# Kernel optimization log

Hardware: AMD Instinct MI355X
Metric: run time of the kernel (lower is better)

The kernel has to match this reference:

```python
import jax, jax.numpy as jnp
import numpy as np

D_MODEL = 1024
NUM_HEADS = 16
HEAD_DIM = D_MODEL // NUM_HEADS


def setup_inputs() -> dict:
    key = jax.random.key(0)
    ks = jax.random.split(key, 9)
    B, S = 4, 2048
    s = 1.0 / np.sqrt(D_MODEL)
    return {
        "x": jax.random.normal(ks[0], (B, S, D_MODEL), dtype=jnp.float32),
        "Wq": jax.random.normal(ks[1], (D_MODEL, D_MODEL), dtype=jnp.float32) * s,
        "bq": jnp.zeros((D_MODEL,), dtype=jnp.float32),
        "Wk": jax.random.normal(ks[2], (D_MODEL, D_MODEL), dtype=jnp.float32) * s,
        "bk": jnp.zeros((D_MODEL,), dtype=jnp.float32),
        "Wv": jax.random.normal(ks[3], (D_MODEL, D_MODEL), dtype=jnp.float32) * s,
        "bv": jnp.zeros((D_MODEL,), dtype=jnp.float32),
        "Wo": jax.random.normal(ks[4], (D_MODEL, D_MODEL), dtype=jnp.float32) * s,
        "bo": jnp.zeros((D_MODEL,), dtype=jnp.float32),
    }


def reference(x, Wq, bq, Wk, bk, Wv, bv, Wo, bo):
    B, S, D = x.shape
    H, Hd = NUM_HEADS, HEAD_DIM
    # projections: [B,S,D] -> [B,H,S,Hd]
    def split_heads(t):
        return t.reshape(B, S, H, Hd).transpose(0, 2, 1, 3)
    q = split_heads(x @ Wq + bq)
    k = split_heads(x @ Wk + bk)
    v = split_heads(x @ Wv + bv)
    scale = 1.0 / jnp.sqrt(jnp.asarray(Hd, dtype=x.dtype))
    scores = jnp.einsum("bhsd,bhtd->bhst", q, k) * scale  # [B,H,S,S]
    attn = jax.nn.softmax(scores, axis=-1)
    ctx = jnp.einsum("bhst,bhtd->bhsd", attn, v)  # [B,H,S,Hd]
    ctx = ctx.transpose(0, 2, 1, 3).reshape(B, S, D)
    return ctx @ Wo + bo
```

## Files before the change

### kernel.cpp

```cpp
#include <hip/hip_runtime.h>
#include <hip/hip_bf16.h>
#include <stdint.h>


typedef __bf16 bf16;
typedef __bf16 bf16x8 __attribute__((ext_vector_type(8)));
typedef float  f32x4  __attribute__((ext_vector_type(4)));
typedef float  f32x8  __attribute__((ext_vector_type(8)));
typedef float  f32x16 __attribute__((ext_vector_type(16)));

#define XB_OFF   (0ull)
#define WT_OFF   (16ull << 20)
#define Q_OFF    (24ull << 20)
#define K_OFF    (40ull << 20)
#define V_OFF    (56ull << 20)
#define CTX_OFF  (72ull << 20)

#define QSCALE 0.18033688011112042591f

__device__ __forceinline__ void gload_lds16(const void* g, void* l) {
  __builtin_amdgcn_global_load_lds(
      (const __attribute__((address_space(1))) void*)g,
      (__attribute__((address_space(3))) void*)l, 16, 0, 0);
}

__global__ __launch_bounds__(256) void cvt_x(const float* __restrict__ x,
                                             bf16* __restrict__ xb) {
  int i = blockIdx.x * 256 + threadIdx.x;
  const float4* p = (const float4*)x;
  float4 a = p[(size_t)i * 2];
  float4 b = p[(size_t)i * 2 + 1];
  bf16x8 o;
  o[0] = (bf16)a.x; o[1] = (bf16)a.y; o[2] = (bf16)a.z; o[3] = (bf16)a.w;
  o[4] = (bf16)b.x; o[5] = (bf16)b.y; o[6] = (bf16)b.z; o[7] = (bf16)b.w;
  *((bf16x8*)xb + i) = o;
}

__global__ __launch_bounds__(256) void cvt_w(const float* __restrict__ w0,
                                             const float* __restrict__ w1,
                                             const float* __restrict__ w2,
                                             const float* __restrict__ w3,
                                             bf16* __restrict__ wt) {
  int z = blockIdx.z;
  const float* W = (z == 0) ? w0 : (z == 1) ? w1 : (z == 2) ? w2 : w3;
  bf16* Wt = wt + (size_t)z * 1024 * 1024;
  __shared__ float tile[64][65];
  int i0 = blockIdx.y * 64, o0 = blockIdx.x * 64;
  int tid = threadIdx.x;
#pragma unroll
  for (int rep = 0; rep < 16; rep++) {
    int idx = rep * 256 + tid;
    int r = idx >> 6, c = idx & 63;
    tile[r][c] = W[(size_t)(i0 + r) * 1024 + o0 + c];
  }
  __syncthreads();
#pragma unroll
  for (int rep = 0; rep < 16; rep++) {
    int idx = rep * 256 + tid;
    int r = idx >> 6, c = idx & 63;
    Wt[(size_t)(o0 + r) * 1024 + i0 + c] = (bf16)tile[c][r];
  }
}

template <int MODE>
__global__ __launch_bounds__(256, 2) void gemm_bt(
    const bf16* __restrict__ A, const bf16* __restrict__ Bt,
    const float* __restrict__ b0, const float* __restrict__ b1,
    const float* __restrict__ b2,
    bf16* __restrict__ Qo, bf16* __restrict__ Ko, bf16* __restrict__ Vo,
    float* __restrict__ out) {
  __shared__ __align__(16) bf16 a_lds[128 * 64];
  __shared__ __align__(16) bf16 b_lds[128 * 64];
  int tid = threadIdx.x;
  int lane = tid & 63, wid = tid >> 6;
  int wr = wid >> 1, wc = wid & 1;
  int g = lane >> 4, rlo = lane & 15;
  int m0 = blockIdx.x * 128, n0 = blockIdx.y * 128;

  f32x4 acc[4][4] = {};
  const char* Ab = (const char*)A;
  const char* Bb = (const char*)Bt;

  for (int k0 = 0; k0 < 1024; k0 += 64) {
#pragma unroll
    for (int rep = 0; rep < 4; rep++) {
      int idx = rep * 256 + tid;
      int row = idx >> 3;
      int sw = ((idx & 7) * 16) ^ ((row & 7) << 4);
      gload_lds16(Ab + ((size_t)(m0 + row) * 1024 + k0) * 2 + sw,
                  (char*)a_lds + (size_t)idx * 16);
    }
#pragma unroll
    for (int rep = 0; rep < 4; rep++) {
      int idx = rep * 256 + tid;
      int row = idx >> 3;
      int sw = ((idx & 7) * 16) ^ ((row & 7) << 4);
      gload_lds16(Bb + ((size_t)(n0 + row) * 1024 + k0) * 2 + sw,
                  (char*)b_lds + (size_t)idx * 16);
    }
    __syncthreads();
#pragma unroll
    for (int ks = 0; ks < 2; ks++) {
      bf16x8 af[4], bfr[4];
#pragma unroll
      for (int mt = 0; mt < 4; mt++) {
        int row = wr * 64 + mt * 16 + rlo;
        int koff = (ks * 32 + g * 8) ^ ((row & 7) << 3);
        af[mt] = *(const bf16x8*)&a_lds[row * 64 + koff];
      }
#pragma unroll
      for (int nt = 0; nt < 4; nt++) {
        int row = wc * 64 + nt * 16 + rlo;
        int koff = (ks * 32 + g * 8) ^ ((row & 7) << 3);
        bfr[nt] = *(const bf16x8*)&b_lds[row * 64 + koff];
      }
#pragma unroll
      for (int mt = 0; mt < 4; mt++)
#pragma unroll
        for (int nt = 0; nt < 4; nt++)
          acc[mt][nt] = __builtin_amdgcn_mfma_f32_16x16x32_bf16(
              af[mt], bfr[nt], acc[mt][nt], 0, 0, 0);
    }
    __syncthreads();
  }

#pragma unroll
  for (int nt = 0; nt < 4; nt++) {
    int n = n0 + wc * 64 + nt * 16 + rlo;
    if (MODE == 0) {
      int which = n >> 10, nn = n & 1023;
      const float* bp = (which == 0) ? b0 : (which == 1) ? b1 : b2;
      float bias = bp[nn];
      bf16* dst = (which == 0) ? Qo : (which == 1) ? Ko : Vo;
      float scale = (which == 0) ? QSCALE : 1.0f;
      int h = nn >> 6, hd = nn & 63;
#pragma unroll
      for (int mt = 0; mt < 4; mt++) {
#pragma unroll
        for (int r = 0; r < 4; r++) {
          int m = m0 + wr * 64 + mt * 16 + g * 4 + r;
          int bb = m >> 11, ss = m & 2047;
          float v = (acc[mt][nt][r] + bias) * scale;
          dst[(((size_t)(bb * 16 + h) * 2048 + ss) << 6) + hd] = (bf16)v;
        }
      }
    } else {
      float bias = b0[n];
#pragma unroll
      for (int mt = 0; mt < 4; mt++) {
#pragma unroll
        for (int r = 0; r < 4; r++) {
          int m = m0 + wr * 64 + mt * 16 + g * 4 + r;
          out[(size_t)m * 1024 + n] = acc[mt][nt][r] + bias;
        }
      }
    }
  }
}

__global__ __launch_bounds__(256) void vtr(const bf16* __restrict__ V,
                                           bf16* __restrict__ Vt) {
  __shared__ bf16 t[64][72];
  int bh = blockIdx.y, s0 = blockIdx.x * 64;
  int tid = threadIdx.x;
  const bf16* Vb = V + ((size_t)bh * 2048 + s0) * 64;
  bf16* Tb = Vt + (size_t)bh * 64 * 2048;
#pragma unroll
  for (int rep = 0; rep < 2; rep++) {
    int idx = rep * 256 + tid;
    int s = idx >> 3, dv = (idx & 7) * 8;
    bf16x8 v = *(const bf16x8*)&Vb[(size_t)s * 64 + dv];
#pragma unroll
    for (int j = 0; j < 8; j++) t[s][dv + j] = v[j];
  }
  __syncthreads();
#pragma unroll
  for (int rep = 0; rep < 2; rep++) {
    int idx = rep * 256 + tid;
    int d = idx >> 3, sc = (idx & 7) * 8;
    bf16x8 v;
#pragma unroll
    for (int j = 0; j < 8; j++) {
      int sl = sc + j;
      int sp = (sl & ~12) | ((sl & 4) << 1) | ((sl & 8) >> 1);
      v[j] = t[sp][d];
    }
    *(bf16x8*)&Tb[(size_t)d * 2048 + s0 + sc] = v;
  }
}

__global__ __launch_bounds__(256, 4) void attn(const bf16* __restrict__ Q,
                                               const bf16* __restrict__ K,
                                               const bf16* __restrict__ Vt,
                                               bf16* __restrict__ ctx) {
  __shared__ __align__(16) bf16 kbuf[2][32 * 64];
  __shared__ __align__(16) bf16 vbuf[2][64 * 64];
  int tid = threadIdx.x;
  int lane = tid & 63, wid = tid >> 6;
  int r31 = lane & 31, half = lane >> 5;
  int wg = blockIdx.x;
  int virt = (wg & 7) * 128 + (wg >> 3);
  int bh = virt >> 4, qt = virt & 15;
  int qbase = qt * 128 + wid * 32;

  const char* Kg = (const char*)(K + (size_t)bh * 2048 * 64);
  const char* Vg = (const char*)(Vt + (size_t)bh * 64 * 2048);

  int srow = lane >> 3;
  int schunk = lane & 7;
  int kt = wid * 8 + srow;
  int ksrc = ((schunk ^ srow) << 4);
  int vd = wid * 8 + srow;
  int vsrc = (((schunk ^ srow) & 3) << 4);

  int rofs[4];
#pragma unroll
  for (int ks = 0; ks < 4; ks++)
    rofs[ks] = r31 * 64 + (((2 * ks + half) ^ (r31 & 7)) << 3);

  const bf16* qrow = Q + ((size_t)bh * 2048 + qbase + r31) * 64 + half * 8;
  bf16x8 qa[4];
#pragma unroll
  for (int ks = 0; ks < 4; ks++) qa[ks] = *(const bf16x8*)&qrow[ks * 16];

  f32x16 o0 = {}, o1 = {};
  f32x8 lvec = {};

#define STAGE(BUF, T0)                                                        \
  do {                                                                        \
    gload_lds16(Kg + ((size_t)((T0) + kt) << 7) + ksrc,                      \
                (char*)kbuf[BUF] + tid * 16);                                 \
    gload_lds16(Vg + ((size_t)vd << 12) + (T0) * 2 + vsrc,                   \
                (char*)vbuf[BUF] + tid * 16);                                 \
    gload_lds16(Vg + ((size_t)(vd + 32) << 12) + (T0) * 2 + vsrc,            \
                (char*)vbuf[BUF] + 4096 + tid * 16);                          \
  } while (0)

  STAGE(0, 0);
  __syncthreads();

  int cur = 0;
  for (int it = 0; it < 64; ++it) {
    STAGE(cur ^ 1, ((it + 1) & 63) * 32);

    const bf16* kb = kbuf[cur];
    const bf16* vb = vbuf[cur];

    f32x16 s = {};
    __builtin_amdgcn_s_setprio(1);
#pragma unroll
    for (int ks = 0; ks < 4; ks++) {
      bf16x8 kf = *(const bf16x8*)&kb[rofs[ks]];
      s = __builtin_amdgcn_mfma_f32_32x32x16_bf16(kf, qa[ks], s, 0, 0, 0);
    }
    __builtin_amdgcn_s_setprio(0);

    bf16x8 v00 = *(const bf16x8*)&vb[rofs[0]];
    bf16x8 v01 = *(const bf16x8*)&vb[rofs[1]];
    bf16x8 v10 = *(const bf16x8*)&vb[2048 + rofs[0]];
    bf16x8 v11 = *(const bf16x8*)&vb[2048 + rofs[1]];

#pragma unroll
    for (int i = 0; i < 16; i++) s[i] = __builtin_amdgcn_exp2f(s[i]);
#pragma unroll
    for (int i = 0; i < 8; i++) lvec[i] += s[i] + s[i + 8];

    bf16x8 pa0, pa1;
#pragma unroll
    for (int i = 0; i < 8; i++) {
      pa0[i] = (bf16)s[i];
      pa1[i] = (bf16)s[8 + i];
    }

    __builtin_amdgcn_s_setprio(1);
    o0 = __builtin_amdgcn_mfma_f32_32x32x16_bf16(pa0, v00, o0, 0, 0, 0);
    o1 = __builtin_amdgcn_mfma_f32_32x32x16_bf16(pa0, v10, o1, 0, 0, 0);
    o0 = __builtin_amdgcn_mfma_f32_32x32x16_bf16(pa1, v01, o0, 0, 0, 0);
    o1 = __builtin_amdgcn_mfma_f32_32x32x16_bf16(pa1, v11, o1, 0, 0, 0);
    __builtin_amdgcn_s_setprio(0);

    __syncthreads();
    cur ^= 1;
  }
#undef STAGE

  float l = (((lvec[0] + lvec[1]) + (lvec[2] + lvec[3])) +
             ((lvec[4] + lvec[5]) + (lvec[6] + lvec[7])));
  l += __shfl_xor(l, 32);
  float inv = 1.0f / l;
  int b = bh >> 4, h = bh & 15;
#pragma unroll
  for (int r = 0; r < 16; r++) {
    int ql = (r & 3) + 8 * (r >> 2) + 4 * half;
    float iv = __shfl(inv, ql);
    size_t base = (((size_t)(b * 2048 + qbase + ql)) << 10) + h * 64 + r31;
    ctx[base] = (bf16)(o0[r] * iv);
    ctx[base + 32] = (bf16)(o1[r] * iv);
  }
}

extern "C" void kernel_launch(void* const* d_in, const int* in_sizes, int n_in,
                              void* d_out, int out_size, void* d_ws, size_t ws_size,
                              hipStream_t stream) {
  const float* x  = (const float*)d_in[0];
  const float* Wq = (const float*)d_in[1];
  const float* bq = (const float*)d_in[2];
  const float* Wk = (const float*)d_in[3];
  const float* bk = (const float*)d_in[4];
  const float* Wv = (const float*)d_in[5];
  const float* bv = (const float*)d_in[6];
  const float* Wo = (const float*)d_in[7];
  const float* bo = (const float*)d_in[8];
  float* out = (float*)d_out;
  char* ws = (char*)d_ws;

  bf16* xb  = (bf16*)(ws + XB_OFF);
  bf16* wt  = (bf16*)(ws + WT_OFF);
  bf16* Qb  = (bf16*)(ws + Q_OFF);
  bf16* Kb  = (bf16*)(ws + K_OFF);
  bf16* Vb  = (bf16*)(ws + V_OFF);
  bf16* cx  = (bf16*)(ws + CTX_OFF);
  bf16* Vtb = (bf16*)(ws + XB_OFF);

  cvt_x<<<4096, 256, 0, stream>>>(x, xb);
  cvt_w<<<dim3(16, 16, 4), 256, 0, stream>>>(Wq, Wk, Wv, Wo, wt);
  gemm_bt<0><<<dim3(64, 24), 256, 0, stream>>>(xb, wt, bq, bk, bv,
                                               Qb, Kb, Vb, nullptr);
  vtr<<<dim3(32, 64), 256, 0, stream>>>(Vb, Vtb);
  attn<<<1024, 256, 0, stream>>>(Qb, Kb, Vtb, cx);
  gemm_bt<1><<<dim3(64, 8), 256, 0, stream>>>(cx, wt + 3ull * 1024 * 1024, bo,
                                              nullptr, nullptr, nullptr,
                                              nullptr, nullptr, out);
}
```

Measured before the change: 180.7 us.

## Triple-buffer K/V tiles with partial vmcnt waits instead of full syncthreads

The attention loop moves from double to triple buffering of the K and V tiles, prefetching two tiles ahead. It replaces __syncthreads with an s_waitcnt vmcnt(2) plus a raw barrier, so one tile's loads can stay in flight across iterations. The V tile layout is shrunk to 64x32 with a new swizzle, which cuts the V stage from two loads to one per thread. The row-sum reduction is also reshaped to four accumulators. LDS use stays the same, and the change relies on the hand-written vmcnt count matching the number of outstanding loads.

```diff
diff --git a/kernel.cpp b/kernel.cpp
--- a/kernel.cpp
+++ b/kernel.cpp
@@ -6,7 +6,6 @@
 typedef __bf16 bf16;
 typedef __bf16 bf16x8 __attribute__((ext_vector_type(8)));
 typedef float  f32x4  __attribute__((ext_vector_type(4)));
-typedef float  f32x8  __attribute__((ext_vector_type(8)));
 typedef float  f32x16 __attribute__((ext_vector_type(16)));
 
 #define XB_OFF   (0ull)
@@ -193,8 +192,8 @@
                                                const bf16* __restrict__ K,
                                                const bf16* __restrict__ Vt,
                                                bf16* __restrict__ ctx) {
-  __shared__ __align__(16) bf16 kbuf[2][32 * 64];
-  __shared__ __align__(16) bf16 vbuf[2][64 * 64];
+  __shared__ __align__(16) bf16 kbuf[3][32 * 64];
+  __shared__ __align__(16) bf16 vbuf[3][64 * 32];
   int tid = threadIdx.x;
   int lane = tid & 63, wid = tid >> 6;
   int r31 = lane & 31, half = lane >> 5;
@@ -206,17 +205,22 @@
   const char* Kg = (const char*)(K + (size_t)bh * 2048 * 64);
   const char* Vg = (const char*)(Vt + (size_t)bh * 64 * 2048);
 
-  int srow = lane >> 3;
-  int schunk = lane & 7;
-  int kt = wid * 8 + srow;
-  int ksrc = ((schunk ^ srow) << 4);
-  int vd = wid * 8 + srow;
-  int vsrc = (((schunk ^ srow) & 3) << 4);
-
-  int rofs[4];
+  int krow = tid >> 3;
+  size_t kofs = (size_t)krow * 128 + (((tid & 7) ^ (krow & 7)) << 4);
+  int vrow = tid >> 2;
+  size_t vofs = (size_t)vrow * 4096 + (((tid & 3) ^ (vrow & 3)) << 4);
+
+  int kread[4];
 #pragma unroll
   for (int ks = 0; ks < 4; ks++)
-    rofs[ks] = r31 * 64 + (((2 * ks + half) ^ (r31 & 7)) << 3);
+    kread[ks] = r31 * 64 + (((2 * ks + half) ^ (r31 & 7)) << 3);
+  int vread[2][2];
+#pragma unroll
+  for (int dh = 0; dh < 2; dh++)
+#pragma unroll
+    for (int ks = 0; ks < 2; ks++)
+      vread[dh][ks] = (dh * 32 + r31) * 32 +
+                      ((((2 * ks + half) & 3) ^ (r31 & 3)) << 3);
 
   const bf16* qrow = Q + ((size_t)bh * 2048 + qbase + r31) * 64 + half * 8;
   bf16x8 qa[4];
@@ -224,46 +228,46 @@
   for (int ks = 0; ks < 4; ks++) qa[ks] = *(const bf16x8*)&qrow[ks * 16];
 
   f32x16 o0 = {}, o1 = {};
-  f32x8 lvec = {};
+  f32x4 lvec = {};
 
 #define STAGE(BUF, T0)                                                        \
   do {                                                                        \
-    gload_lds16(Kg + ((size_t)((T0) + kt) << 7) + ksrc,                      \
-                (char*)kbuf[BUF] + tid * 16);                                 \
-    gload_lds16(Vg + ((size_t)vd << 12) + (T0) * 2 + vsrc,                   \
-                (char*)vbuf[BUF] + tid * 16);                                 \
-    gload_lds16(Vg + ((size_t)(vd + 32) << 12) + (T0) * 2 + vsrc,            \
-                (char*)vbuf[BUF] + 4096 + tid * 16);                          \
+    gload_lds16(Kg + (size_t)(T0) * 128 + kofs, (char*)kbuf[BUF] + tid * 16); \
+    gload_lds16(Vg + (size_t)(T0) * 2 + vofs, (char*)vbuf[BUF] + tid * 16);   \
   } while (0)
 
   STAGE(0, 0);
-  __syncthreads();
-
-  int cur = 0;
+  STAGE(1, 32);
+  asm volatile("s_waitcnt vmcnt(2)" ::: "memory");
+  __builtin_amdgcn_s_barrier();
+
+  int cs = 0;
   for (int it = 0; it < 64; ++it) {
-    STAGE(cur ^ 1, ((it + 1) & 63) * 32);
-
-    const bf16* kb = kbuf[cur];
-    const bf16* vb = vbuf[cur];
+    int sb = cs + 2 - ((cs >= 1) ? 3 : 0);
+    STAGE(sb, ((it + 2) & 63) * 32);
+
+    const bf16* kb = kbuf[cs];
+    const bf16* vb = vbuf[cs];
 
     f32x16 s = {};
     __builtin_amdgcn_s_setprio(1);
 #pragma unroll
     for (int ks = 0; ks < 4; ks++) {
-      bf16x8 kf = *(const bf16x8*)&kb[rofs[ks]];
+      bf16x8 kf = *(const bf16x8*)&kb[kread[ks]];
       s = __builtin_amdgcn_mfma_f32_32x32x16_bf16(kf, qa[ks], s, 0, 0, 0);
     }
     __builtin_amdgcn_s_setprio(0);
 
-    bf16x8 v00 = *(const bf16x8*)&vb[rofs[0]];
-    bf16x8 v01 = *(const bf16x8*)&vb[rofs[1]];
-    bf16x8 v10 = *(const bf16x8*)&vb[2048 + rofs[0]];
-    bf16x8 v11 = *(const bf16x8*)&vb[2048 + rofs[1]];
+    bf16x8 v00 = *(const bf16x8*)&vb[vread[0][0]];
+    bf16x8 v01 = *(const bf16x8*)&vb[vread[0][1]];
+    bf16x8 v10 = *(const bf16x8*)&vb[vread[1][0]];
+    bf16x8 v11 = *(const bf16x8*)&vb[vread[1][1]];
 
 #pragma unroll
     for (int i = 0; i < 16; i++) s[i] = __builtin_amdgcn_exp2f(s[i]);
 #pragma unroll
-    for (int i = 0; i < 8; i++) lvec[i] += s[i] + s[i + 8];
+    for (int i = 0; i < 4; i++)
+      lvec[i] += (s[i] + s[i + 4]) + (s[i + 8] + s[i + 12]);
 
     bf16x8 pa0, pa1;
 #pragma unroll
@@ -274,18 +278,19 @@
 
     __builtin_amdgcn_s_setprio(1);
     o0 = __builtin_amdgcn_mfma_f32_32x32x16_bf16(pa0, v00, o0, 0, 0, 0);
+    o0 = __builtin_amdgcn_mfma_f32_32x32x16_bf16(pa1, v01, o0, 0, 0, 0);
     o1 = __builtin_amdgcn_mfma_f32_32x32x16_bf16(pa0, v10, o1, 0, 0, 0);
-    o0 = __builtin_amdgcn_mfma_f32_32x32x16_bf16(pa1, v01, o0, 0, 0, 0);
     o1 = __builtin_amdgcn_mfma_f32_32x32x16_bf16(pa1, v11, o1, 0, 0, 0);
     __builtin_amdgcn_s_setprio(0);
 
-    __syncthreads();
-    cur ^= 1;
+    asm volatile("s_waitcnt vmcnt(2)" ::: "memory");
+    __builtin_amdgcn_s_barrier();
+
+    cs = (cs == 2) ? 0 : cs + 1;
   }
 #undef STAGE
 
-  float l = (((lvec[0] + lvec[1]) + (lvec[2] + lvec[3])) +
-             ((lvec[4] + lvec[5]) + (lvec[6] + lvec[7])));
+  float l = (lvec[0] + lvec[1]) + (lvec[2] + lvec[3]);
   l += __shfl_xor(l, 32);
   float inv = 1.0f / l;
   int b = bh >> 4, h = bh & 15;
```

Measured after the change: 180.2 us. About the same (-0.3%).
